# Optimization experiments

Measured on AMD Instinct MI355X. Metric: run time of the kernel, lower is better.

Reference implementation:

```python
import jax, jax.numpy as jnp
import numpy as np

IN_CH, OUT_CH, HIDDEN_FREQ, M1, M2 = 32, 32, 64, 32, 32
B, H, W = 8, 256, 256


def setup_inputs() -> dict:
    key = jax.random.key(0)
    k1, k2, k3, k4, k5 = jax.random.split(key, 5)
    scale = 1.0 / (IN_CH * OUT_CH)
    x = jax.random.normal(k1, (B, IN_CH, H, W), dtype=jnp.float32)
    mod1 = jax.random.normal(k2, (B, 1, 1, M1, M2, 2), dtype=jnp.float32)
    mod2 = jax.random.normal(k3, (B, 1, 1, M1, M2, 2), dtype=jnp.float32)
    weights = scale * jax.random.uniform(k4, (IN_CH, OUT_CH, 2, HIDDEN_FREQ), dtype=jnp.float32)
    # torch Linear(hidden_freq, m1*m2*2, bias=False): weight (m1*m2*2, hidden_freq)
    lim = 1.0 / np.sqrt(HIDDEN_FREQ)
    mlp_w = jax.random.uniform(k5, (M1 * M2 * 2, HIDDEN_FREQ), dtype=jnp.float32, minval=-lim, maxval=lim)
    return {"x": x, "mod1": mod1, "mod2": mod2, "weights": weights, "mlp_w": mlp_w}


def reference(x, mod1, mod2, weights, mlp_w):
    Bn, Ci, Hn, Wn = x.shape
    Co = weights.shape[1]
    x_ft = jnp.fft.rfft2(x)  # (B, Ci, H, W//2+1) complex
    # MLP-generated spectral weights: (Ci, Co, 2, hidden) @ (hidden, m1*m2*2)
    w = (weights @ mlp_w.T).reshape(Ci, Co, 2, M1, M2, 2)
    wc = jax.lax.complex(w[..., 0], w[..., 1])        # (Ci, Co, 2, M1, M2)
    mod1c = jax.lax.complex(mod1[..., 0], mod1[..., 1])  # (B,1,1,M1,M2)
    mod2c = jax.lax.complex(mod2[..., 0], mod2[..., 1])
    cm1 = wc[:, :, 0] * mod1c  # (B, Ci, Co, M1, M2)
    cm2 = wc[:, :, 1] * mod2c
    out1 = jnp.einsum('bixy,bioxy->boxy', x_ft[:, :, :M1, :M2], cm1)
    out2 = jnp.einsum('bixy,bioxy->boxy', x_ft[:, :, -M1:, :M2], cm2)
    out_ft = jnp.zeros((Bn, Co, Hn, Wn // 2 + 1), dtype=x_ft.dtype)
    out_ft = out_ft.at[:, :, :M1, :M2].set(out1)
    out_ft = out_ft.at[:, :, -M1:, :M2].set(out2)
    return jnp.fft.irfft2(out_ft, s=(Hn, Wn))
```

## Files before the change

kernel.cpp:

```cpp
#include <hip/hip_runtime.h>

#define BB 8
#define CI 32
#define CO 32
#define HH 256
#define WW 256
#define HF 64
#define KX 32
#define NJ 64

typedef __attribute__((ext_vector_type(8))) short short8;
typedef __attribute__((ext_vector_type(4))) float f32x4;

__device__ __constant__ float PI2 = 6.28318530717958647692f;

__device__ inline unsigned short f2bf(float f) {
    unsigned u = __float_as_uint(f);
    u += 0x7FFF + ((u >> 16) & 1);
    return (unsigned short)(u >> 16);
}
__device__ inline void splitbf(float f, unsigned short& h, unsigned short& l) {
    unsigned short hh = f2bf(f);
    float fh = __uint_as_float(((unsigned)hh) << 16);
    l = f2bf(f - fh);
    h = hh;
}

__global__ void kprep(unsigned short* __restrict__ pk) {
    int id = blockIdx.x * 256 + threadIdx.x;
    if (id < 16384) {
        int j = id & 7, lane = (id >> 3) & 63, nt = (id >> 9) & 3, kt = id >> 11;
        int k = kt * 32 + (lane >> 4) * 8 + j;
        int n = nt * 16 + (lane & 15);
        int kx = n >> 1, c = n & 1;
        int p = (k * kx) & 255;
        float sn, cs; sincosf(PI2 * (float)p / 256.0f, &sn, &cs);
        float val = c ? -sn : cs;
        unsigned short h, l; splitbf(val, h, l);
        pk[id] = h; pk[id + 16384] = l;
    } else {
        int id2 = id - 16384;
        int j = id2 & 7, lane = (id2 >> 3) & 63, nt = (id2 >> 9) & 15, kt = id2 >> 13;
        int k = kt * 32 + (lane >> 4) * 8 + j;
        int w = nt * 16 + (lane & 15);
        int kx = k >> 1, c = k & 1;
        int p = (kx * w) & 255;
        float sn, cs; sincosf(PI2 * (float)p / 256.0f, &sn, &cs);
        float ck = (kx == 0) ? 1.0f : 2.0f;
        float val = c ? -ck * sn : ck * cs;
        unsigned short h, l; splitbf(val, h, l);
        pk[id2 + 32768] = h; pk[id2 + 49152] = l;
    }
}

__global__ __launch_bounds__(256) void kweights(const float* __restrict__ wts,
                                                const float* __restrict__ mlp,
                                                float* __restrict__ WC) {
    int t = threadIdx.x;
    int wid = t >> 6, lane = t & 63;
    int bm = blockIdx.x >> 4, bn = blockIdx.x & 15;
    int m0 = bm * 128 + (wid >> 1) * 64;
    int n0 = bn * 128 + (wid & 1) * 64;
    int l15 = lane & 15, lq = lane >> 4;

    f32x4 acc[4][4];
    #pragma unroll
    for (int mt = 0; mt < 4; mt++)
        #pragma unroll
        for (int nt = 0; nt < 4; nt++)
            acc[mt][nt] = (f32x4){0.f, 0.f, 0.f, 0.f};

    #pragma unroll
    for (int kt = 0; kt < 2; kt++) {
        short8 Ah[4], Al[4];
        #pragma unroll
        for (int mt = 0; mt < 4; mt++) {
            int m = m0 + mt * 16 + l15;
            int c = m >> 10, mm = m & 1023;
            const float4* p = (const float4*)(mlp + (mm * 2 + c) * 64 + kt * 32 + lq * 8);
            float4 v0 = p[0], v1 = p[1];
            float vals[8] = {v0.x, v0.y, v0.z, v0.w, v1.x, v1.y, v1.z, v1.w};
            #pragma unroll
            for (int e = 0; e < 8; e++) {
                unsigned short h, l; splitbf(vals[e], h, l);
                Ah[mt][e] = (short)h; Al[mt][e] = (short)l;
            }
        }
        #pragma unroll
        for (int nt = 0; nt < 4; nt++) {
            int n = n0 + nt * 16 + l15;
            int s = n >> 10, io = n & 1023;
            const float4* p = (const float4*)(wts + (io * 2 + s) * 64 + kt * 32 + lq * 8);
            float4 v0 = p[0], v1 = p[1];
            float vals[8] = {v0.x, v0.y, v0.z, v0.w, v1.x, v1.y, v1.z, v1.w};
            short8 Bh, Bl;
            #pragma unroll
            for (int e = 0; e < 8; e++) {
                unsigned short h, l; splitbf(vals[e], h, l);
                Bh[e] = (short)h; Bl[e] = (short)l;
            }
            #pragma unroll
            for (int mt = 0; mt < 4; mt++) {
                acc[mt][nt] = __builtin_amdgcn_mfma_f32_16x16x32_bf16(Ah[mt], Bh, acc[mt][nt], 0, 0, 0);
                acc[mt][nt] = __builtin_amdgcn_mfma_f32_16x16x32_bf16(Ah[mt], Bl, acc[mt][nt], 0, 0, 0);
                acc[mt][nt] = __builtin_amdgcn_mfma_f32_16x16x32_bf16(Al[mt], Bh, acc[mt][nt], 0, 0, 0);
            }
        }
    }
    #pragma unroll
    for (int mt = 0; mt < 4; mt++)
        #pragma unroll
        for (int nt = 0; nt < 4; nt++)
            #pragma unroll
            for (int r = 0; r < 4; r++) {
                int m = m0 + mt * 16 + lq * 4 + r;
                int n = n0 + nt * 16 + l15;
                int addr = (((n >> 10) * 1024 + (m & 1023)) * 2 + (m >> 10)) * 1024 + (n & 1023);
                WC[addr] = acc[mt][nt][r];
            }
}

__global__ __launch_bounds__(512) void kfwd(const float* __restrict__ x,
                                            const unsigned short* __restrict__ pk,
                                            float* __restrict__ F) {
    __shared__ float xs[HH * 64];
    int t = threadIdx.x;
    int bi = blockIdx.x;
    int w = t >> 6, lane = t & 63;
    int l15 = lane & 15, lq = lane >> 4;

    f32x4 acc[2][4];
    #pragma unroll
    for (int mt = 0; mt < 2; mt++)
        #pragma unroll
        for (int nt = 0; nt < 4; nt++)
            acc[mt][nt] = (f32x4){0.f, 0.f, 0.f, 0.f};

    #pragma unroll
    for (int kt = 0; kt < 8; kt++) {
        short8 bh[4], bl[4];
        #pragma unroll
        for (int nt = 0; nt < 4; nt++) {
            bh[nt] = *(const short8*)(pk + ((size_t)((kt * 4 + nt) * 64 + lane)) * 8);
            bl[nt] = *(const short8*)(pk + 16384 + ((size_t)((kt * 4 + nt) * 64 + lane)) * 8);
        }
        #pragma unroll
        for (int mt = 0; mt < 2; mt++) {
            const float4* ap = (const float4*)(x + (size_t)(bi * 256 + w * 32 + mt * 16 + l15) * 256 + kt * 32 + lq * 8);
            float4 v0 = ap[0], v1 = ap[1];
            float vals[8] = {v0.x, v0.y, v0.z, v0.w, v1.x, v1.y, v1.z, v1.w};
            short8 ah, al;
            #pragma unroll
            for (int e = 0; e < 8; e++) {
                unsigned short h, l; splitbf(vals[e], h, l);
                ah[e] = (short)h; al[e] = (short)l;
            }
            #pragma unroll
            for (int nt = 0; nt < 4; nt++) {
                acc[mt][nt] = __builtin_amdgcn_mfma_f32_16x16x32_bf16(ah, bh[nt], acc[mt][nt], 0, 0, 0);
                acc[mt][nt] = __builtin_amdgcn_mfma_f32_16x16x32_bf16(ah, bl[nt], acc[mt][nt], 0, 0, 0);
                acc[mt][nt] = __builtin_amdgcn_mfma_f32_16x16x32_bf16(al, bh[nt], acc[mt][nt], 0, 0, 0);
            }
        }
    }
    #pragma unroll
    for (int mt = 0; mt < 2; mt++)
        #pragma unroll
        for (int nt = 0; nt < 4; nt++)
            #pragma unroll
            for (int r = 0; r < 4; r++)
                xs[(w * 32 + mt * 16 + lq * 4 + r) * 64 + nt * 16 + l15] = acc[mt][nt][r];
    __syncthreads();

    int j = lane;
    int ky = (j < 32) ? j : (192 + j);
    float sn, cs;
    sincosf(-PI2 * (float)ky / 256.0f, &sn, &cs);
    float tr = 1.f, ti = 0.f;
    float ar[4], ai[4];
    #pragma unroll
    for (int q = 0; q < 4; q++) { ar[q] = 0.f; ai[q] = 0.f; }
    #pragma unroll 4
    for (int h = 0; h < HH; h++) {
        #pragma unroll
        for (int q = 0; q < 4; q++) {
            float2 v = *(const float2*)&xs[h * 64 + (w * 4 + q) * 2];
            ar[q] = fmaf(v.x, tr, ar[q]); ar[q] = fmaf(-v.y, ti, ar[q]);
            ai[q] = fmaf(v.x, ti, ai[q]); ai[q] = fmaf(v.y, tr, ai[q]);
        }
        float ntr = tr * cs - ti * sn;
        ti = fmaf(tr, sn, ti * cs);
        tr = ntr;
    }
    float2* Fo = ((float2*)F) + ((size_t)bi * NJ + j) * KX + w * 4;
    #pragma unroll
    for (int q = 0; q < 4; q++) Fo[q] = make_float2(ar[q], ai[q]);
}

__global__ void kmodes(const float* __restrict__ F, const float* __restrict__ WC,
                       const float* __restrict__ mod1, const float* __restrict__ mod2,
                       float* __restrict__ OM) {
    int m = blockIdx.x;
    int j = m >> 5, kx = m & 31;
    int s = j >> 5;
    int m1 = j & 31, m2 = kx;
    __shared__ float2 fs[BB][CI];
    __shared__ float wcr[CI * CO];
    __shared__ float wci[CI * CO];
    int t = threadIdx.x;
    {
        int b = t >> 5, i = t & 31;
        fs[b][i] = ((const float2*)F)[((size_t)(b * CI + i) * NJ + j) * KX + kx];
    }
    {
        const float4* wg = (const float4*)(WC + ((size_t)(s * 1024 + m1 * 32 + m2) * 2) * 1024);
        ((float4*)wcr)[t] = wg[t];
        ((float4*)wci)[t] = wg[t + 256];
    }
    __syncthreads();
    int b = t >> 5, o = t & 31;
    float ar = 0.f, ai = 0.f;
    #pragma unroll 8
    for (int i = 0; i < CI; i++) {
        float2 f = fs[b][i];
        float wx = wcr[i * 32 + o];
        float wy = wci[i * 32 + o];
        ar = fmaf(f.x, wx, ar);
        ar = fmaf(-f.y, wy, ar);
        ai = fmaf(f.x, wy, ai);
        ai = fmaf(f.y, wx, ai);
    }
    const float* mp = (s == 0) ? mod1 : mod2;
    float mr = mp[(b * 1024 + m1 * 32 + m2) * 2 + 0];
    float mi = mp[(b * 1024 + m1 * 32 + m2) * 2 + 1];
    const float scale = 1.0f / 65536.0f;
    float outr = (ar * mr - ai * mi) * scale;
    float outi = (ar * mi + ai * mr) * scale;
    ((float2*)OM)[((size_t)(b * CO + o) * NJ + j) * KX + kx] = make_float2(outr, outi);
}

__global__ __launch_bounds__(512) void kinv(const float* __restrict__ OM,
                                            const unsigned short* __restrict__ pk,
                                            float* __restrict__ y) {
    __shared__ float smem[16384];
    float2* os = (float2*)smem;
    int t = threadIdx.x;
    int bo = blockIdx.x;
    {
        const float4* src = (const float4*)OM + (size_t)bo * 1024;
        ((float4*)smem)[t] = src[t];
        ((float4*)smem)[t + 512] = src[t + 512];
    }
    __syncthreads();

    int h = t & 255, half = t >> 8;
    float sn, cs;
    sincosf(PI2 * (float)h / 256.0f, &sn, &cs);
    float tr = 1.f, ti = 0.f;
    float accr[16], acci[16];
    #pragma unroll
    for (int q = 0; q < 16; q++) { accr[q] = 0.f; acci[q] = 0.f; }
    for (int j = 0; j < NJ; j++) {
        if (j == 32) ti = -ti;
        #pragma unroll
        for (int q = 0; q < 16; q++) {
            float2 v = os[j * 32 + half * 16 + q];
            accr[q] = fmaf(v.x, tr, accr[q]);
            accr[q] = fmaf(-v.y, ti, accr[q]);
            acci[q] = fmaf(v.x, ti, acci[q]);
            acci[q] = fmaf(v.y, tr, acci[q]);
        }
        float ntr = tr * cs - ti * sn;
        ti = fmaf(tr, sn, ti * cs);
        tr = ntr;
    }
    __syncthreads();
    #pragma unroll
    for (int q = 0; q < 16; q++) {
        int kx = half * 16 + q;
        *(float2*)&smem[(kx >> 2) * 2048 + h * 8 + ((2 * kx) & 6)] = make_float2(accr[q], acci[q]);
    }
    __syncthreads();

    int w = t >> 6, lane = t & 63;
    int l15 = lane & 15, lq = lane >> 4;
    const unsigned short* pkD = pk + 32768;
    short8 Bh[2][2], Bl[2][2];
    #pragma unroll
    for (int kt = 0; kt < 2; kt++)
        #pragma unroll
        for (int ntl = 0; ntl < 2; ntl++) {
            int nt = w * 2 + ntl;
            Bh[kt][ntl] = *(const short8*)(pkD + ((size_t)((kt * 16 + nt) * 64 + lane)) * 8);
            Bl[kt][ntl] = *(const short8*)(pkD + 16384 + ((size_t)((kt * 16 + nt) * 64 + lane)) * 8);
        }
    #pragma unroll 4
    for (int mt = 0; mt < 16; mt++) {
        f32x4 acc2[2];
        acc2[0] = (f32x4){0.f, 0.f, 0.f, 0.f};
        acc2[1] = (f32x4){0.f, 0.f, 0.f, 0.f};
        #pragma unroll
        for (int kt = 0; kt < 2; kt++) {
            const float* ap = &smem[(kt * 4 + lq) * 2048 + (mt * 16 + l15) * 8];
            short8 ah, al;
            #pragma unroll
            for (int e = 0; e < 8; e++) {
                unsigned short hh, ll; splitbf(ap[e], hh, ll);
                ah[e] = (short)hh; al[e] = (short)ll;
            }
            #pragma unroll
            for (int ntl = 0; ntl < 2; ntl++) {
                acc2[ntl] = __builtin_amdgcn_mfma_f32_16x16x32_bf16(ah, Bh[kt][ntl], acc2[ntl], 0, 0, 0);
                acc2[ntl] = __builtin_amdgcn_mfma_f32_16x16x32_bf16(ah, Bl[kt][ntl], acc2[ntl], 0, 0, 0);
                acc2[ntl] = __builtin_amdgcn_mfma_f32_16x16x32_bf16(al, Bh[kt][ntl], acc2[ntl], 0, 0, 0);
            }
        }
        #pragma unroll
        for (int ntl = 0; ntl < 2; ntl++)
            #pragma unroll
            for (int r = 0; r < 4; r++)
                y[(size_t)(bo * 256 + mt * 16 + lq * 4 + r) * 256 + (w * 2 + ntl) * 16 + l15] = acc2[ntl][r];
    }
}

extern "C" void kernel_launch(void* const* d_in, const int* in_sizes, int n_in,
                              void* d_out, int out_size, void* d_ws, size_t ws_size,
                              hipStream_t stream) {
    const float* x    = (const float*)d_in[0];
    const float* mod1 = (const float*)d_in[1];
    const float* mod2 = (const float*)d_in[2];
    const float* wts  = (const float*)d_in[3];
    const float* mlp  = (const float*)d_in[4];
    float* y = (float*)d_out;

    float* ws = (float*)d_ws;
    float* F  = ws;
    float* WC = F + 1048576;
    float* OM = WC + 4194304;
    unsigned short* pk = (unsigned short*)(OM + 1048576);

    kprep   <<<dim3(128),  dim3(256), 0, stream>>>(pk);
    kweights<<<dim3(256),  dim3(256), 0, stream>>>(wts, mlp, WC);
    kfwd    <<<dim3(BB * CI), dim3(512), 0, stream>>>(x, pk, F);
    kmodes  <<<dim3(NJ * KX), dim3(256), 0, stream>>>(F, WC, mod1, mod2, OM);
    kinv    <<<dim3(BB * CO), dim3(512), 0, stream>>>(OM, pk, y);
}
```

Baseline: 198.5 us.

## Replace scalar twiddle-recurrence DFT stages with split-bf16 MFMA matmuls

Result: faster. 166.5 us (-16.1%).

```diff
diff --git a/kernel.cpp b/kernel.cpp
--- a/kernel.cpp
+++ b/kernel.cpp
@@ -13,6 +13,12 @@
 typedef __attribute__((ext_vector_type(4))) float f32x4;
 
 __device__ __constant__ float PI2 = 6.28318530717958647692f;
+
+#define PK_E   0
+#define PK_D   32768
+#define PK_TF  65536
+#define PK_A2  131072
+#define PK_TOTAL 196608
 
 __device__ inline unsigned short f2bf(float f) {
     unsigned u = __float_as_uint(f);
@@ -38,7 +44,7 @@
         float val = c ? -sn : cs;
         unsigned short h, l; splitbf(val, h, l);
         pk[id] = h; pk[id + 16384] = l;
-    } else {
+    } else if (id < 32768) {
         int id2 = id - 16384;
         int j = id2 & 7, lane = (id2 >> 3) & 63, nt = (id2 >> 9) & 15, kt = id2 >> 13;
         int k = kt * 32 + (lane >> 4) * 8 + j;
@@ -49,7 +55,31 @@
         float ck = (kx == 0) ? 1.0f : 2.0f;
         float val = c ? -ck * sn : ck * cs;
         unsigned short h, l; splitbf(val, h, l);
-        pk[id2 + 32768] = h; pk[id2 + 49152] = l;
+        pk[PK_D + id2] = h; pk[PK_D + 16384 + id2] = l;
+    } else if (id < 65536) {
+        int idt = id - 32768;
+        int e = idt & 7, lane = (idt >> 3) & 63, kt = (idt >> 9) & 7, mt = (idt >> 12) & 3, p = (idt >> 14) & 1;
+        int j = mt * 16 + (lane & 15);
+        int h = kt * 32 + (lane >> 4) * 8 + e;
+        int ky = (j < 32) ? j : (192 + j);
+        int ang = (ky * h) & 255;
+        float sn, cs; sincosf(PI2 * (float)ang / 256.0f, &sn, &cs);
+        float val = p ? sn : cs;
+        unsigned short hh, ll; splitbf(val, hh, ll);
+        int base = PK_TF + p * 32768 + mt * 4096 + kt * 512 + lane * 8 + e;
+        pk[base] = hh; pk[base + 16384] = ll;
+    } else {
+        int ida = id - 65536;
+        int e = ida & 7, lane = (ida >> 3) & 63, kt = (ida >> 9) & 3, mt = ida >> 11;
+        int h = mt * 16 + (lane & 15);
+        int kp = kt * 32 + (lane >> 4) * 8 + e;
+        int j = kp & 63, p = kp >> 6;
+        int ky = (j < 32) ? j : (192 + j);
+        int ang = (ky * h) & 255;
+        float sn, cs; sincosf(PI2 * (float)ang / 256.0f, &sn, &cs);
+        float val = p ? sn : cs;
+        unsigned short hh, ll; splitbf(val, hh, ll);
+        pk[PK_A2 + ida] = hh; pk[PK_A2 + 32768 + ida] = ll;
     }
 }
 
@@ -120,10 +150,11 @@
             }
 }
 
+#define XS_STR 264
 __global__ __launch_bounds__(512) void kfwd(const float* __restrict__ x,
                                             const unsigned short* __restrict__ pk,
                                             float* __restrict__ F) {
-    __shared__ float xs[HH * 64];
+    __shared__ short Xbf[2][64 * XS_STR];
     int t = threadIdx.x;
     int bi = blockIdx.x;
     int w = t >> 6, lane = t & 63;
@@ -168,33 +199,51 @@
         #pragma unroll
         for (int nt = 0; nt < 4; nt++)
             #pragma unroll
-            for (int r = 0; r < 4; r++)
-                xs[(w * 32 + mt * 16 + lq * 4 + r) * 64 + nt * 16 + l15] = acc[mt][nt][r];
+            for (int r = 0; r < 4; r++) {
+                int hrow = w * 32 + mt * 16 + lq * 4 + r;
+                int n = nt * 16 + l15;
+                unsigned short hh, ll; splitbf(acc[mt][nt][r], hh, ll);
+                Xbf[0][n * XS_STR + hrow] = (short)hh;
+                Xbf[1][n * XS_STR + hrow] = (short)ll;
+            }
     __syncthreads();
 
-    int j = lane;
-    int ky = (j < 32) ? j : (192 + j);
-    float sn, cs;
-    sincosf(-PI2 * (float)ky / 256.0f, &sn, &cs);
-    float tr = 1.f, ti = 0.f;
-    float ar[4], ai[4];
-    #pragma unroll
-    for (int q = 0; q < 4; q++) { ar[q] = 0.f; ai[q] = 0.f; }
-    #pragma unroll 4
-    for (int h = 0; h < HH; h++) {
-        #pragma unroll
-        for (int q = 0; q < 4; q++) {
-            float2 v = *(const float2*)&xs[h * 64 + (w * 4 + q) * 2];
-            ar[q] = fmaf(v.x, tr, ar[q]); ar[q] = fmaf(-v.y, ti, ar[q]);
-            ai[q] = fmaf(v.x, ti, ai[q]); ai[q] = fmaf(v.y, tr, ai[q]);
-        }
-        float ntr = tr * cs - ti * sn;
-        ti = fmaf(tr, sn, ti * cs);
-        tr = ntr;
-    }
-    float2* Fo = ((float2*)F) + ((size_t)bi * NJ + j) * KX + w * 4;
-    #pragma unroll
-    for (int q = 0; q < 4; q++) Fo[q] = make_float2(ar[q], ai[q]);
+    int mtq = w >> 1, ntbase = (w & 1) * 2;
+    f32x4 ca[2], cb[2];
+    ca[0] = (f32x4){0.f,0.f,0.f,0.f}; ca[1] = (f32x4){0.f,0.f,0.f,0.f};
+    cb[0] = (f32x4){0.f,0.f,0.f,0.f}; cb[1] = (f32x4){0.f,0.f,0.f,0.f};
+    #pragma unroll
+    for (int kt = 0; kt < 8; kt++) {
+        int aoff = PK_TF + mtq * 4096 + kt * 512 + lane * 8;
+        short8 Ach = *(const short8*)(pk + aoff);
+        short8 Acl = *(const short8*)(pk + aoff + 16384);
+        short8 Ash = *(const short8*)(pk + aoff + 32768);
+        short8 Asl = *(const short8*)(pk + aoff + 49152);
+        #pragma unroll
+        for (int ntl = 0; ntl < 2; ntl++) {
+            int n = (ntbase + ntl) * 16 + l15;
+            short8 xh = *(const short8*)&Xbf[0][n * XS_STR + kt * 32 + lq * 8];
+            short8 xl = *(const short8*)&Xbf[1][n * XS_STR + kt * 32 + lq * 8];
+            ca[ntl] = __builtin_amdgcn_mfma_f32_16x16x32_bf16(Ach, xh, ca[ntl], 0, 0, 0);
+            ca[ntl] = __builtin_amdgcn_mfma_f32_16x16x32_bf16(Ach, xl, ca[ntl], 0, 0, 0);
+            ca[ntl] = __builtin_amdgcn_mfma_f32_16x16x32_bf16(Acl, xh, ca[ntl], 0, 0, 0);
+            cb[ntl] = __builtin_amdgcn_mfma_f32_16x16x32_bf16(Ash, xh, cb[ntl], 0, 0, 0);
+            cb[ntl] = __builtin_amdgcn_mfma_f32_16x16x32_bf16(Ash, xl, cb[ntl], 0, 0, 0);
+            cb[ntl] = __builtin_amdgcn_mfma_f32_16x16x32_bf16(Asl, xh, cb[ntl], 0, 0, 0);
+        }
+    }
+    #pragma unroll
+    for (int ntl = 0; ntl < 2; ntl++) {
+        int n = (ntbase + ntl) * 16 + l15;
+        #pragma unroll
+        for (int r = 0; r < 4; r++) {
+            float a = ca[ntl][r];
+            float bsw = __shfl_xor(cb[ntl][r], 1, 64);
+            float out = (n & 1) ? (a - bsw) : (a + bsw);
+            int j = mtq * 16 + lq * 4 + r;
+            F[(size_t)bi * 4096 + j * 64 + n] = out;
+        }
+    }
 }
 
 __global__ void kmodes(const float* __restrict__ F, const float* __restrict__ WC,
@@ -239,52 +288,92 @@
     ((float2*)OM)[((size_t)(b * CO + o) * NJ + j) * KX + kx] = make_float2(outr, outi);
 }
 
+#define BP_STR 136
+#define GB_STR 72
 __global__ __launch_bounds__(512) void kinv(const float* __restrict__ OM,
                                             const unsigned short* __restrict__ pk,
                                             float* __restrict__ y) {
-    __shared__ float smem[16384];
-    float2* os = (float2*)smem;
+    __shared__ short smem[2 * 256 * GB_STR];
+    short* Bp0 = smem;
+    short* Bp1 = smem + 64 * BP_STR;
+    short* G0 = smem;
+    short* G1 = smem + 256 * GB_STR;
     int t = threadIdx.x;
     int bo = blockIdx.x;
+    int lane = t & 63, w = t >> 6;
+    int l15 = lane & 15, lq = lane >> 4;
+
     {
         const float4* src = (const float4*)OM + (size_t)bo * 1024;
-        ((float4*)smem)[t] = src[t];
-        ((float4*)smem)[t + 512] = src[t + 512];
+        #pragma unroll
+        for (int q = 0; q < 2; q++) {
+            int idx4 = t + q * 512;
+            float4 v = src[idx4];
+            #pragma unroll
+            for (int half = 0; half < 2; half++) {
+                int e = idx4 * 2 + half;
+                int j = e >> 5, kx = e & 31;
+                float Or = half ? v.z : v.x;
+                float Oi = half ? v.w : v.y;
+                unsigned short orh, orl, oih, oil, nih, nil;
+                splitbf(Or, orh, orl);
+                splitbf(Oi, oih, oil);
+                splitbf(-Oi, nih, nil);
+                Bp0[(2 * kx) * BP_STR + j] = (short)orh;      Bp1[(2 * kx) * BP_STR + j] = (short)orl;
+                Bp0[(2 * kx) * BP_STR + 64 + j] = (short)nih; Bp1[(2 * kx) * BP_STR + 64 + j] = (short)nil;
+                Bp0[(2 * kx + 1) * BP_STR + j] = (short)oih;  Bp1[(2 * kx + 1) * BP_STR + j] = (short)oil;
+                Bp0[(2 * kx + 1) * BP_STR + 64 + j] = (short)orh; Bp1[(2 * kx + 1) * BP_STR + 64 + j] = (short)orl;
+            }
+        }
     }
     __syncthreads();
 
-    int h = t & 255, half = t >> 8;
-    float sn, cs;
-    sincosf(PI2 * (float)h / 256.0f, &sn, &cs);
-    float tr = 1.f, ti = 0.f;
-    float accr[16], acci[16];
-    #pragma unroll
-    for (int q = 0; q < 16; q++) { accr[q] = 0.f; acci[q] = 0.f; }
-    for (int j = 0; j < NJ; j++) {
-        if (j == 32) ti = -ti;
-        #pragma unroll
-        for (int q = 0; q < 16; q++) {
-            float2 v = os[j * 32 + half * 16 + q];
-            accr[q] = fmaf(v.x, tr, accr[q]);
-            accr[q] = fmaf(-v.y, ti, accr[q]);
-            acci[q] = fmaf(v.x, ti, acci[q]);
-            acci[q] = fmaf(v.y, tr, acci[q]);
-        }
-        float ntr = tr * cs - ti * sn;
-        ti = fmaf(tr, sn, ti * cs);
-        tr = ntr;
+    f32x4 g[2][4];
+    #pragma unroll
+    for (int mtl = 0; mtl < 2; mtl++)
+        #pragma unroll
+        for (int nt = 0; nt < 4; nt++)
+            g[mtl][nt] = (f32x4){0.f, 0.f, 0.f, 0.f};
+    #pragma unroll
+    for (int kt = 0; kt < 4; kt++) {
+        short8 a2h[2], a2l[2];
+        #pragma unroll
+        for (int mtl = 0; mtl < 2; mtl++) {
+            int mt = w * 2 + mtl;
+            int aoff = PK_A2 + mt * 2048 + kt * 512 + lane * 8;
+            a2h[mtl] = *(const short8*)(pk + aoff);
+            a2l[mtl] = *(const short8*)(pk + aoff + 32768);
+        }
+        #pragma unroll
+        for (int nt = 0; nt < 4; nt++) {
+            int n = nt * 16 + l15;
+            short8 bh = *(const short8*)&Bp0[n * BP_STR + kt * 32 + lq * 8];
+            short8 bl = *(const short8*)&Bp1[n * BP_STR + kt * 32 + lq * 8];
+            #pragma unroll
+            for (int mtl = 0; mtl < 2; mtl++) {
+                g[mtl][nt] = __builtin_amdgcn_mfma_f32_16x16x32_bf16(a2h[mtl], bh, g[mtl][nt], 0, 0, 0);
+                g[mtl][nt] = __builtin_amdgcn_mfma_f32_16x16x32_bf16(a2h[mtl], bl, g[mtl][nt], 0, 0, 0);
+                g[mtl][nt] = __builtin_amdgcn_mfma_f32_16x16x32_bf16(a2l[mtl], bh, g[mtl][nt], 0, 0, 0);
+            }
+        }
     }
     __syncthreads();
-    #pragma unroll
-    for (int q = 0; q < 16; q++) {
-        int kx = half * 16 + q;
-        *(float2*)&smem[(kx >> 2) * 2048 + h * 8 + ((2 * kx) & 6)] = make_float2(accr[q], acci[q]);
-    }
+
+    #pragma unroll
+    for (int mtl = 0; mtl < 2; mtl++)
+        #pragma unroll
+        for (int nt = 0; nt < 4; nt++)
+            #pragma unroll
+            for (int r = 0; r < 4; r++) {
+                int h = (w * 2 + mtl) * 16 + lq * 4 + r;
+                int n = nt * 16 + l15;
+                unsigned short hh, ll; splitbf(g[mtl][nt][r], hh, ll);
+                G0[h * GB_STR + n] = (short)hh;
+                G1[h * GB_STR + n] = (short)ll;
+            }
     __syncthreads();
 
-    int w = t >> 6, lane = t & 63;
-    int l15 = lane & 15, lq = lane >> 4;
-    const unsigned short* pkD = pk + 32768;
+    const unsigned short* pkD = pk + PK_D;
     short8 Bh[2][2], Bl[2][2];
     #pragma unroll
     for (int kt = 0; kt < 2; kt++)
@@ -301,13 +390,8 @@
         acc2[1] = (f32x4){0.f, 0.f, 0.f, 0.f};
         #pragma unroll
         for (int kt = 0; kt < 2; kt++) {
-            const float* ap = &smem[(kt * 4 + lq) * 2048 + (mt * 16 + l15) * 8];
-            short8 ah, al;
-            #pragma unroll
-            for (int e = 0; e < 8; e++) {
-                unsigned short hh, ll; splitbf(ap[e], hh, ll);
-                ah[e] = (short)hh; al[e] = (short)ll;
-            }
+            short8 ah = *(const short8*)&G0[(mt * 16 + l15) * GB_STR + kt * 32 + lq * 8];
+            short8 al = *(const short8*)&G1[(mt * 16 + l15) * GB_STR + kt * 32 + lq * 8];
             #pragma unroll
             for (int ntl = 0; ntl < 2; ntl++) {
                 acc2[ntl] = __builtin_amdgcn_mfma_f32_16x16x32_bf16(ah, Bh[kt][ntl], acc2[ntl], 0, 0, 0);
@@ -339,7 +423,7 @@
     float* OM = WC + 4194304;
     unsigned short* pk = (unsigned short*)(OM + 1048576);
 
-    kprep   <<<dim3(128),  dim3(256), 0, stream>>>(pk);
+    kprep   <<<dim3(384),  dim3(256), 0, stream>>>(pk);
     kweights<<<dim3(256),  dim3(256), 0, stream>>>(wts, mlp, WC);
     kfwd    <<<dim3(BB * CI), dim3(512), 0, stream>>>(x, pk, F);
     kmodes  <<<dim3(NJ * KX), dim3(256), 0, stream>>>(F, WC, mod1, mod2, OM);
```
